# Kernel optimization log

Measured on AMD Instinct MI355X. Metric: run time of the kernel, lower is better.

The kernel has to match this reference:

```python
import jax, jax.numpy as jnp
import numpy as np

N, E, B, D, L = 100000, 600000, 128, 128, 3
BOT = 64
EPS = 1e-5


def _forward(query_x, corpus_x, gin_eps, mlp_W1, mlp_b1, mlp_W2, mlp_b2, bn_gamma, bn_beta,
             pool_G1, pool_g1b, pool_G2, pool_g2b, pool_Wm,
             int_G1, int_g1b, int_G2, int_g2b, int_F1, int_f1b, int_F2, int_f2b,
             sc_G1, sc_g1b, sc_G2, sc_g2b, sc_F1, sc_f1b, sc_F2, sc_f2b,
             query_edge_index, query_graph_idx, corpus_edge_index, corpus_graph_idx, num_graphs):
    def gin(x, ei, l):
        # GINConv: sum of source-node features into targets, plus (1+eps)*self
        agg = jax.ops.segment_sum(x[ei[0]], ei[1], num_segments=x.shape[0])
        h = (1.0 + gin_eps[l]) * x + agg
        h = jax.nn.relu(h @ mlp_W1[l] + mlp_b1[l]) @ mlp_W2[l] + mlp_b2[l]
        mu = h.mean(axis=0)
        var = ((h - mu) ** 2).mean(axis=0)  # biased var (BatchNorm training mode)
        h = (h - mu) * jax.lax.rsqrt(var + EPS) * bn_gamma[l] + bn_beta[l]
        return jax.nn.relu(h)  # dropout p=0.0

    def pool(x, gidx, l):
        coef = jnp.tanh(jax.nn.relu(x @ pool_G1[l] + pool_g1b[l]) @ pool_G2[l] + pool_g2b[l])
        s = (coef + 1.0) * x
        sums = jax.ops.segment_sum(s, gidx, num_segments=num_graphs)
        cnt = jax.ops.segment_sum(jnp.ones((x.shape[0],), x.dtype), gidx, num_segments=num_graphs)
        mean = sums / cnt[:, None]
        gc = jnp.tanh(mean @ pool_Wm[l])  # [B, D]
        node_coef = jax.nn.sigmoid(jnp.sum(s * gc[gidx], axis=1))  # [N]
        return jax.ops.segment_sum(node_coef[:, None] * s, gidx, num_segments=num_graphs)

    def interact(q, c, l):
        comb = jnp.concatenate([q, c], axis=1)  # [B, 2D]
        coef = jax.nn.sigmoid(jax.nn.relu(comb @ int_G1[l] + int_g1b[l]) @ int_G2[l] + int_g2b[l])
        sc = (coef + 1.0) * comb
        return jax.nn.relu(jax.nn.relu(sc @ int_F1[l] + int_f1b[l]) @ int_F2[l] + int_f2b[l])

    qx, cx = query_x, corpus_x
    feats = []
    for l in range(gin_eps.shape[0]):
        qx = gin(qx, query_edge_index, l)
        cx = gin(cx, corpus_edge_index, l)
        feats.append(interact(pool(qx, query_graph_idx, l), pool(cx, corpus_graph_idx, l), l))
    f = jnp.concatenate(feats, axis=1)  # [B, sum(filters)//2]
    coef = jax.nn.sigmoid(jax.nn.relu(f @ sc_G1 + sc_g1b) @ sc_G2 + sc_g2b)
    sf = (coef + 1.0) * f
    return (jax.nn.relu(sf @ sc_F1 + sc_f1b) @ sc_F2 + sc_f2b).squeeze(-1)  # [B]


def setup_inputs() -> dict:
    key = jax.random.key(0)
    kit = iter(jax.random.split(key, 64))
    def nrm(shape, s=0.05):
        return jax.random.normal(next(kit), shape, jnp.float32) * s
    C, R, OUT, AGG, RG = 2 * D, (2 * D) // 4, D // 2, (3 * D) // 2, ((3 * D) // 2) // 4
    inp = {
        "query_x": nrm((N, D), 1.0),
        "query_edge_index": jax.random.randint(next(kit), (2, E), 0, N),
        "query_graph_idx": jnp.sort(jax.random.randint(next(kit), (N,), 0, B)),
        "corpus_x": nrm((N, D), 1.0),
        "corpus_edge_index": jax.random.randint(next(kit), (2, E), 0, N),
        "corpus_graph_idx": jnp.sort(jax.random.randint(next(kit), (N,), 0, B)),
        "num_graphs": B,
        "gin_eps": jnp.zeros((L,), jnp.float32),
        "mlp_W1": nrm((L, D, D)), "mlp_b1": jnp.zeros((L, D)),
        "mlp_W2": nrm((L, D, D)), "mlp_b2": jnp.zeros((L, D)),
        "bn_gamma": jnp.ones((L, D)), "bn_beta": jnp.zeros((L, D)),
        "pool_G1": nrm((L, D, D // 4)), "pool_g1b": jnp.zeros((L, D // 4)),
        "pool_G2": nrm((L, D // 4, D)), "pool_g2b": jnp.zeros((L, D)),
        "pool_Wm": nrm((L, D, D)),
        "int_G1": nrm((L, C, R)), "int_g1b": jnp.zeros((L, R)),
        "int_G2": nrm((L, R, C)), "int_g2b": jnp.zeros((L, C)),
        "int_F1": nrm((L, C, C)), "int_f1b": jnp.zeros((L, C)),
        "int_F2": nrm((L, C, OUT)), "int_f2b": jnp.zeros((L, OUT)),
        "sc_G1": nrm((AGG, RG)), "sc_g1b": jnp.zeros((RG,)),
        "sc_G2": nrm((RG, AGG)), "sc_g2b": jnp.zeros((AGG,)),
        "sc_F1": nrm((AGG, BOT)), "sc_f1b": jnp.zeros((BOT,)),
        "sc_F2": nrm((BOT, 1)), "sc_f2b": jnp.zeros((1,)),
    }
    return inp


def reference(query_x, query_edge_index, query_graph_idx, corpus_x, corpus_edge_index, corpus_graph_idx,
              num_graphs, gin_eps, mlp_W1, mlp_b1, mlp_W2, mlp_b2, bn_gamma, bn_beta,
              pool_G1, pool_g1b, pool_G2, pool_g2b, pool_Wm,
              int_G1, int_g1b, int_G2, int_g2b, int_F1, int_f1b, int_F2, int_f2b,
              sc_G1, sc_g1b, sc_G2, sc_g2b, sc_F1, sc_f1b, sc_F2, sc_f2b):
    return _forward(query_x, corpus_x, gin_eps, mlp_W1, mlp_b1, mlp_W2, mlp_b2, bn_gamma, bn_beta,
                    pool_G1, pool_g1b, pool_G2, pool_g2b, pool_Wm,
                    int_G1, int_g1b, int_G2, int_g2b, int_F1, int_f1b, int_F2, int_f2b,
                    sc_G1, sc_g1b, sc_G2, sc_g2b, sc_F1, sc_f1b, sc_F2, sc_f2b,
                    query_edge_index, query_graph_idx, corpus_edge_index, corpus_graph_idx, num_graphs)
```

## Files before the change

### kernel.cpp

```cpp
#include <hip/hip_runtime.h>
#include <hip/hip_bf16.h>

constexpr int NN  = 100000;
constexpr int NN2 = 200000;
constexpr int NE  = 600000;
constexpr int NB  = 128;
constexpr int D   = 128;
constexpr int NL  = 3;
constexpr int CAP = 48;
constexpr int MT_TOT = NN2 / 16;
constexpr int MT_Q   = NN / 16;

typedef __bf16 bf16x8 __attribute__((ext_vector_type(8)));
typedef float f32x4 __attribute__((ext_vector_type(4)));
typedef unsigned short us8 __attribute__((ext_vector_type(8)));

__device__ __forceinline__ float sigmoidf_(float x) { return 1.0f / (1.0f + __expf(-x)); }
__device__ __forceinline__ unsigned short f2b(float f) {
    __hip_bfloat16 h = __float2bfloat16(f);
    return __builtin_bit_cast(unsigned short, h);
}
__device__ __forceinline__ float b2f(unsigned short u) {
    __hip_bfloat16 h = __builtin_bit_cast(__hip_bfloat16, u);
    return __bfloat162float(h);
}
__device__ __forceinline__ bf16x8 ldfrag(const unsigned short* p) {
    return __builtin_bit_cast(bf16x8, *(const us8*)p);
}

__global__ __launch_bounds__(256) void k_csr_fill(const int* __restrict__ qei, const int* __restrict__ cei,
                                                  int* __restrict__ deg, int* __restrict__ bucket) {
    int e = blockIdx.x * 256 + threadIdx.x;
    int src, dst;
    if (e < NE) {
        src = qei[e]; dst = qei[NE + e];
    } else if (e < 2 * NE) {
        src = cei[e - NE] + NN; dst = cei[NE + (e - NE)] + NN;
    } else return;
    int pos = atomicAdd(&deg[dst], 1);
    if (pos < CAP) bucket[(size_t)dst * CAP + pos] = src;
}

__global__ __launch_bounds__(256) void k_cnt(const int* __restrict__ gq, const int* __restrict__ gc,
                                             float* __restrict__ cnt) {
    __shared__ float h[256];
    for (int i = threadIdx.x; i < 256; i += 256) h[i] = 0.f;
    __syncthreads();
    int total = gridDim.x * 256;
    int tid = blockIdx.x * 256 + threadIdx.x;
    int per = (NN2 + total - 1) / total;
    int r0 = tid * per, r1 = min(r0 + per, NN2);
    if (r0 < r1) {
        int cur = (r0 < NN) ? gq[r0] : 128 + gc[r0 - NN];
        float c = 0.f;
        for (int r = r0; r < r1; ++r) {
            int g = (r < NN) ? gq[r] : 128 + gc[r - NN];
            if (g != cur) { atomicAdd(&h[cur], c); c = 0.f; cur = g; }
            c += 1.f;
        }
        atomicAdd(&h[cur], c);
    }
    __syncthreads();
    for (int i = threadIdx.x; i < 256; i += 256)
        if (h[i] != 0.f) atomicAdd(&cnt[i], h[i]);
}

__global__ __launch_bounds__(256) void k_wprep_all(
    const float* mW1, const float* mW2, const float* pG1, const float* pG2,
    const float* iG1, const float* iG2, const float* iF1, const float* iF2,
    const float* sG1, const float* sG2, const float* sF1,
    unsigned short* W1t, unsigned short* W2t, unsigned short* G1t, unsigned short* G2t,
    unsigned short* iG1t, unsigned short* iG2t, unsigned short* iF1t, unsigned short* iF2t,
    unsigned short* sG1t, unsigned short* sG2t, unsigned short* sF1t) {
    int i = blockIdx.x * 256 + threadIdx.x;
#define SEG(CNT, KK, NN_, SRC, DST)                                              \
    if (i < (CNT)) {                                                             \
        int l = i / ((KK) * (NN_)), r = i % ((KK) * (NN_));                      \
        int n = r / (KK), k = r % (KK);                                          \
        DST[i] = f2b(SRC[(size_t)l * (KK) * (NN_) + (size_t)k * (NN_) + n]);     \
        return;                                                                  \
    }                                                                            \
    i -= (CNT);
    SEG(49152, 128, 128, mW1, W1t)
    SEG(49152, 128, 128, mW2, W2t)
    SEG(12288, 128, 32, pG1, G1t)
    SEG(12288, 32, 128, pG2, G2t)
    SEG(49152, 256, 64, iG1, iG1t)
    SEG(49152, 64, 256, iG2, iG2t)
    SEG(196608, 256, 256, iF1, iF1t)
    SEG(49152, 256, 64, iF2, iF2t)
    SEG(9216, 192, 48, sG1, sG1t)
    if (i < 12288) {
        int n = i / 64, k = i % 64;
        sG2t[i] = (k < 48) ? f2b(sG2[(size_t)k * 192 + n]) : (unsigned short)0;
        return;
    }
    i -= 12288;
    SEG(12288, 192, 64, sF1, sF1t)
#undef SEG
}

template <bool BF16IN>
__global__ __launch_bounds__(256) void k_gather(const float* __restrict__ qx, const float* __restrict__ cx,
                                                const unsigned short* __restrict__ xb, unsigned short* __restrict__ z,
                                                const int* __restrict__ deg, const int* __restrict__ bucket,
                                                const float* __restrict__ eps_p, int l) {
    int r = blockIdx.x * 16 + (threadIdx.x >> 4);
    int c8 = threadIdx.x & 15;
    float e = 1.0f + eps_p[l];
    float a[8];
    const float* base = nullptr; int off = 0;
    if constexpr (BF16IN) {
        us8 v = *(const us8*)(xb + (size_t)r * D + c8 * 8);
#pragma unroll
        for (int j = 0; j < 8; ++j) a[j] = e * b2f(v[j]);
    } else {
        base = (r < NN) ? qx : cx; off = (r < NN) ? 0 : NN;
        float4 v0 = *(const float4*)(base + (size_t)(r - off) * D + c8 * 8);
        float4 v1 = *(const float4*)(base + (size_t)(r - off) * D + c8 * 8 + 4);
        a[0] = e * v0.x; a[1] = e * v0.y; a[2] = e * v0.z; a[3] = e * v0.w;
        a[4] = e * v1.x; a[5] = e * v1.y; a[6] = e * v1.z; a[7] = e * v1.w;
    }
    int d = deg[r]; d = (d < CAP) ? d : CAP;
    const int* bk = bucket + (size_t)r * CAP;
    int i = 0;
    for (; i + 4 <= d; i += 4) {
        int s0 = bk[i], s1 = bk[i + 1], s2 = bk[i + 2], s3 = bk[i + 3];
        if constexpr (BF16IN) {
            us8 u0 = *(const us8*)(xb + (size_t)s0 * D + c8 * 8);
            us8 u1 = *(const us8*)(xb + (size_t)s1 * D + c8 * 8);
            us8 u2 = *(const us8*)(xb + (size_t)s2 * D + c8 * 8);
            us8 u3 = *(const us8*)(xb + (size_t)s3 * D + c8 * 8);
#pragma unroll
            for (int j = 0; j < 8; ++j)
                a[j] += b2f(u0[j]) + b2f(u1[j]) + b2f(u2[j]) + b2f(u3[j]);
        } else {
            const float* p0 = base + (size_t)(s0 - off) * D + c8 * 8;
            const float* p1 = base + (size_t)(s1 - off) * D + c8 * 8;
            const float* p2 = base + (size_t)(s2 - off) * D + c8 * 8;
            const float* p3 = base + (size_t)(s3 - off) * D + c8 * 8;
            float4 w0 = *(const float4*)p0, w0b = *(const float4*)(p0 + 4);
            float4 w1 = *(const float4*)p1, w1b = *(const float4*)(p1 + 4);
            float4 w2 = *(const float4*)p2, w2b = *(const float4*)(p2 + 4);
            float4 w3 = *(const float4*)p3, w3b = *(const float4*)(p3 + 4);
            a[0] += w0.x + w1.x + w2.x + w3.x; a[1] += w0.y + w1.y + w2.y + w3.y;
            a[2] += w0.z + w1.z + w2.z + w3.z; a[3] += w0.w + w1.w + w2.w + w3.w;
            a[4] += w0b.x + w1b.x + w2b.x + w3b.x; a[5] += w0b.y + w1b.y + w2b.y + w3b.y;
            a[6] += w0b.z + w1b.z + w2b.z + w3b.z; a[7] += w0b.w + w1b.w + w2b.w + w3b.w;
        }
    }
    for (; i < d; ++i) {
        int s0 = bk[i];
        if constexpr (BF16IN) {
            us8 u0 = *(const us8*)(xb + (size_t)s0 * D + c8 * 8);
#pragma unroll
            for (int j = 0; j < 8; ++j) a[j] += b2f(u0[j]);
        } else {
            const float* p0 = base + (size_t)(s0 - off) * D + c8 * 8;
            float4 w0 = *(const float4*)p0, w0b = *(const float4*)(p0 + 4);
            a[0] += w0.x; a[1] += w0.y; a[2] += w0.z; a[3] += w0.w;
            a[4] += w0b.x; a[5] += w0b.y; a[6] += w0b.z; a[7] += w0b.w;
        }
    }
    us8 o;
#pragma unroll
    for (int j = 0; j < 8; ++j) o[j] = f2b(a[j]);
    *(us8*)(z + (size_t)r * D + c8 * 8) = o;
}

constexpr int HSTR = 136;
__global__ __launch_bounds__(256, 2) void k_mlp(unsigned short* zh,
                                                const unsigned short* __restrict__ W1t,
                                                const unsigned short* __restrict__ W2t,
                                                const float* __restrict__ b1,
                                                const float* __restrict__ b2,
                                                float* __restrict__ stat) {
    __shared__ unsigned short hb[2][2][16 * HSTR];
    __shared__ float red[512];
    int wave = threadIdx.x >> 6, lane = threadIdx.x & 63;
    int col16 = lane & 15, quad = lane >> 4;
    int g = wave >> 1, half = wave & 1;
    bf16x8 bf1[4][4], bf2[4][4];
    float bb1[4], bb2[4];
#pragma unroll
    for (int t = 0; t < 4; ++t) {
        int c = half * 64 + t * 16 + col16;
        bb1[t] = b1[c]; bb2[t] = b2[c];
#pragma unroll
        for (int kc = 0; kc < 4; ++kc) {
            bf1[t][kc] = ldfrag(W1t + (size_t)c * D + kc * 32 + quad * 8);
            bf2[t][kc] = ldfrag(W2t + (size_t)c * D + kc * 32 + quad * 8);
        }
    }
    float cs[2][4] = {{0.f,0.f,0.f,0.f},{0.f,0.f,0.f,0.f}};
    float cq[2][4] = {{0.f,0.f,0.f,0.f},{0.f,0.f,0.f,0.f}};
    int groups = gridDim.x * 2;
    int iters = (MT_TOT + groups - 1) / groups;
    for (int n = 0; n < iters; ++n) {
        int mt = blockIdx.x * 2 + g + n * groups;
        bool act = (mt < MT_TOT);
        int pp = n & 1;
        unsigned short* hbuf = hb[pp][g];
        {
            const unsigned short* Ap = zh + ((size_t)(act ? mt : 0) * 16 + col16) * D + quad * 8;
            f32x4 acc[4];
#pragma unroll
            for (int t = 0; t < 4; ++t) acc[t] = (f32x4){0.f, 0.f, 0.f, 0.f};
#pragma unroll
            for (int kc = 0; kc < 4; ++kc) {
                bf16x8 af = ldfrag(Ap + kc * 32);
#pragma unroll
                for (int t = 0; t < 4; ++t)
                    acc[t] = __builtin_amdgcn_mfma_f32_16x16x32_bf16(af, bf1[t][kc], acc[t], 0, 0, 0);
            }
#pragma unroll
            for (int t = 0; t < 4; ++t) {
                int c = half * 64 + t * 16 + col16;
#pragma unroll
                for (int r = 0; r < 4; ++r)
                    hbuf[(quad * 4 + r) * HSTR + c] = f2b(fmaxf(acc[t][r] + bb1[t], 0.f));
            }
        }
        __syncthreads();
        {
            f32x4 acc[4];
#pragma unroll
            for (int t = 0; t < 4; ++t) acc[t] = (f32x4){0.f, 0.f, 0.f, 0.f};
#pragma unroll
            for (int kc = 0; kc < 4; ++kc) {
                bf16x8 af = ldfrag(&hbuf[col16 * HSTR + kc * 32 + quad * 8]);
#pragma unroll
                for (int t = 0; t < 4; ++t)
                    acc[t] = __builtin_amdgcn_mfma_f32_16x16x32_bf16(af, bf2[t][kc], acc[t], 0, 0, 0);
            }
            if (act) {
                int side = (mt < MT_Q) ? 0 : 1;
#pragma unroll
                for (int t = 0; t < 4; ++t) {
                    int c = half * 64 + t * 16 + col16;
#pragma unroll
                    for (int r = 0; r < 4; ++r) {
                        int m = mt * 16 + quad * 4 + r;
                        float v = acc[t][r] + bb2[t];
                        zh[(size_t)m * D + c] = f2b(v);
                        cs[side][t] += v; cq[side][t] += v * v;
                    }
                }
            }
        }
    }
    for (int i = threadIdx.x; i < 512; i += 256) red[i] = 0.f;
    __syncthreads();
#pragma unroll
    for (int t = 0; t < 4; ++t) {
        int c = half * 64 + t * 16 + col16;
#pragma unroll
        for (int side = 0; side < 2; ++side) {
            atomicAdd(&red[side * 256 + c], cs[side][t]);
            atomicAdd(&red[side * 256 + 128 + c], cq[side][t]);
        }
    }
    __syncthreads();
    for (int i = threadIdx.x; i < 512; i += 256) atomicAdd(&stat[i], red[i]);
}

__global__ __launch_bounds__(256, 2) void k_pool(const unsigned short* __restrict__ H,
                                                 const unsigned short* __restrict__ G1t,
                                                 const unsigned short* __restrict__ G2t,
                                                 const float* __restrict__ b1,
                                                 const float* __restrict__ b2,
                                                 const float* __restrict__ stat,
                                                 const float* __restrict__ gamma,
                                                 const float* __restrict__ beta,
                                                 const int* __restrict__ gq, const int* __restrict__ gcix,
                                                 unsigned short* __restrict__ Xo,
                                                 unsigned short* __restrict__ S,
                                                 float* __restrict__ seg_sum) {
    __shared__ float sc_s[256], sh_s[256];
    __shared__ unsigned short xt[4][16 * HSTR];
    __shared__ unsigned short t2t[4][16 * 40];
    {
        int t = threadIdx.x, side = t >> 7, c = t & 127;
        const float invN = 1.0f / (float)NN;
        float mu = stat[side * 256 + c] * invN;
        float var = fmaxf(stat[side * 256 + 128 + c] * invN - mu * mu, 0.f);
        float inv = rsqrtf(var + 1e-5f);
        float s = gamma[c] * inv;
        sc_s[t] = s;
        sh_s[t] = beta[c] - mu * s;
    }
    __syncthreads();
    int wave = threadIdx.x >> 6, lane = threadIdx.x & 63;
    int col16 = lane & 15, quad = lane >> 4;
    unsigned short* xtile = xt[wave];
    unsigned short* t2tile = t2t[wave];
    int nwaves = gridDim.x * 4;
    int per = (MT_TOT + nwaves - 1) / nwaves;
    int wid = blockIdx.x * 4 + wave;
    int mt0 = wid * per, mt1 = min(mt0 + per, MT_TOT);
    if (mt0 >= mt1) return;

    bf16x8 g1f[2][4], g2f[8];
    float bb1[2], bb2[8];
#pragma unroll
    for (int t = 0; t < 2; ++t) {
        int c = t * 16 + col16;
        bb1[t] = b1[c];
#pragma unroll
        for (int kc = 0; kc < 4; ++kc)
            g1f[t][kc] = ldfrag(G1t + (size_t)c * D + kc * 32 + quad * 8);
    }
#pragma unroll
    for (int t = 0; t < 8; ++t) {
        int c = t * 16 + col16;
        bb2[t] = b2[c];
        g2f[t] = ldfrag(G2t + (size_t)c * 32 + quad * 8);
    }
    float sacc[8] = {0.f, 0.f, 0.f, 0.f, 0.f, 0.f, 0.f, 0.f};
    int curg = -1;
    for (int mt = mt0; mt < mt1; ++mt) {
        int side = (mt < MT_Q) ? 0 : 1;
        const float* scp = sc_s + side * 128;
        const float* shp = sh_s + side * 128;
        const unsigned short* Hp = H + ((size_t)mt * 16 + col16) * D + quad * 8;
        unsigned short* Xp = Xo + ((size_t)mt * 16 + col16) * D + quad * 8;
        f32x4 acc1[2];
#pragma unroll
        for (int t = 0; t < 2; ++t) acc1[t] = (f32x4){0.f, 0.f, 0.f, 0.f};
#pragma unroll
        for (int kc = 0; kc < 4; ++kc) {
            us8 hv = *(const us8*)(Hp + kc * 32);
            int k0 = kc * 32 + quad * 8;
            float4 s0 = *(const float4*)&scp[k0], s1 = *(const float4*)&scp[k0 + 4];
            float4 h0 = *(const float4*)&shp[k0], h1 = *(const float4*)&shp[k0 + 4];
            us8 xv;
            xv[0] = f2b(fmaxf(b2f(hv[0]) * s0.x + h0.x, 0.f));
            xv[1] = f2b(fmaxf(b2f(hv[1]) * s0.y + h0.y, 0.f));
            xv[2] = f2b(fmaxf(b2f(hv[2]) * s0.z + h0.z, 0.f));
            xv[3] = f2b(fmaxf(b2f(hv[3]) * s0.w + h0.w, 0.f));
            xv[4] = f2b(fmaxf(b2f(hv[4]) * s1.x + h1.x, 0.f));
            xv[5] = f2b(fmaxf(b2f(hv[5]) * s1.y + h1.y, 0.f));
            xv[6] = f2b(fmaxf(b2f(hv[6]) * s1.z + h1.z, 0.f));
            xv[7] = f2b(fmaxf(b2f(hv[7]) * s1.w + h1.w, 0.f));
            *(us8*)(Xp + kc * 32) = xv;
            *(us8*)(xtile + col16 * HSTR + k0) = xv;
            bf16x8 af = __builtin_bit_cast(bf16x8, xv);
#pragma unroll
            for (int t = 0; t < 2; ++t)
                acc1[t] = __builtin_amdgcn_mfma_f32_16x16x32_bf16(af, g1f[t][kc], acc1[t], 0, 0, 0);
        }
#pragma unroll
        for (int t = 0; t < 2; ++t) {
            int c = t * 16 + col16;
#pragma unroll
            for (int r = 0; r < 4; ++r)
                t2tile[(quad * 4 + r) * 40 + c] = f2b(fmaxf(acc1[t][r] + bb1[t], 0.f));
        }
        bf16x8 af2 = ldfrag(t2tile + col16 * 40 + quad * 8);
        f32x4 acc2[8];
#pragma unroll
        for (int t = 0; t < 8; ++t) {
            acc2[t] = (f32x4){0.f, 0.f, 0.f, 0.f};
            acc2[t] = __builtin_amdgcn_mfma_f32_16x16x32_bf16(af2, g2f[t], acc2[t], 0, 0, 0);
        }
#pragma unroll
        for (int r = 0; r < 4; ++r) {
            int m = mt * 16 + quad * 4 + r;
            int g = (m < NN) ? gq[m] : 128 + gcix[m - NN];
            if (g != curg) {
                if (curg >= 0) {
#pragma unroll
                    for (int t = 0; t < 8; ++t) {
                        atomicAdd(&seg_sum[(size_t)curg * D + t * 16 + col16], sacc[t]);
                        sacc[t] = 0.f;
                    }
                }
                curg = g;
            }
#pragma unroll
            for (int t = 0; t < 8; ++t) {
                int c = t * 16 + col16;
                float v = (tanhf(acc2[t][r] + bb2[t]) + 1.f) * b2f(xtile[(quad * 4 + r) * HSTR + c]);
                S[(size_t)m * D + c] = f2b(v);
                sacc[t] += v;
            }
        }
    }
    if (curg >= 0) {
#pragma unroll
        for (int t = 0; t < 8; ++t)
            atomicAdd(&seg_sum[(size_t)curg * D + t * 16 + col16], sacc[t]);
    }
}

__global__ void k_gc(const float* __restrict__ sums, const float* __restrict__ cnt,
                     const float* __restrict__ Wm, float* __restrict__ gc) {
    __shared__ float m[D];
    int b = blockIdx.x, j = threadIdx.x;
    m[j] = sums[b * D + j] / cnt[b];
    __syncthreads();
    float a = 0.f;
#pragma unroll 8
    for (int i = 0; i < D; ++i) a += m[i] * Wm[i * D + j];
    gc[b * D + j] = tanhf(a);
}

__global__ __launch_bounds__(256) void k_ncseg(const unsigned short* __restrict__ S,
                                               const int* __restrict__ gq, const int* __restrict__ gc,
                                               const float* __restrict__ gcb,
                                               float* __restrict__ dq, float* __restrict__ dc) {
    int stream = blockIdx.x * 4 + (threadIdx.x >> 6);
    int lane = threadIdx.x & 63;
    int nstream = gridDim.x * 4;
    int per = (NN2 + nstream - 1) / nstream;
    int r0 = stream * per;
    int r1 = min(r0 + per, NN2);
    if (r0 >= r1) return;
    float a0 = 0.f, a1 = 0.f;
    int cur = (r0 < NN) ? gq[r0] : 128 + gc[r0 - NN];
    for (int r = r0; r < r1; ++r) {
        int g = (r < NN) ? gq[r] : 128 + gc[r - NN];
        if (g != cur) {
            float* base = (cur < 128) ? (dq + cur * D) : (dc + (cur - 128) * D);
            atomicAdd(&base[lane * 2], a0);
            atomicAdd(&base[lane * 2 + 1], a1);
            a0 = 0.f; a1 = 0.f; cur = g;
        }
        ushort2 sv = *(const ushort2*)&S[(size_t)r * D + lane * 2];
        float2 gv = *(const float2*)&gcb[(size_t)g * D + lane * 2];
        float v0 = b2f(sv.x), v1 = b2f(sv.y);
        float p = v0 * gv.x + v1 * gv.y;
#pragma unroll
        for (int off = 1; off < 64; off <<= 1) p += __shfl_xor(p, off, 64);
        float nc = sigmoidf_(p);
        a0 += nc * v0; a1 += nc * v1;
    }
    float* base = (cur < 128) ? (dq + cur * D) : (dc + (cur - 128) * D);
    atomicAdd(&base[lane * 2], a0);
    atomicAdd(&base[lane * 2 + 1], a1);
}

constexpr int LSTR = 264;
__global__ __launch_bounds__(256) void k_interact(const float* __restrict__ pooled,
                                                  const unsigned short* __restrict__ iG1t, const float* __restrict__ ig1b,
                                                  const unsigned short* __restrict__ iG2t, const float* __restrict__ ig2b,
                                                  const unsigned short* __restrict__ iF1t, const float* __restrict__ if1b,
                                                  const unsigned short* __restrict__ iF2t, const float* __restrict__ if2b,
                                                  unsigned short* __restrict__ featsb) {
    __shared__ unsigned short bufC[16 * LSTR];
    __shared__ unsigned short bufA[16 * LSTR];
    __shared__ unsigned short bufB[16 * LSTR];
    int t = threadIdx.x, wave = t >> 6, lane = t & 63;
    int col16 = lane & 15, quad = lane >> 4;
    int pg = blockIdx.x & 7, l = blockIdx.x >> 3;
    int p0 = pg * 16;
    {
        int r = t >> 4, c0 = (t & 15) * 16;
        const float* src = (c0 < 128)
            ? (pooled + (size_t)l * NB * D + (size_t)(p0 + r) * D + c0)
            : (pooled + (size_t)(NL + l) * NB * D + (size_t)(p0 + r) * D + (c0 - 128));
#pragma unroll
        for (int j = 0; j < 16; ++j) bufC[r * LSTR + c0 + j] = f2b(src[j]);
    }
    __syncthreads();
    {
        f32x4 acc = (f32x4){0.f, 0.f, 0.f, 0.f};
        int n = wave * 16 + col16;
#pragma unroll
        for (int kc = 0; kc < 8; ++kc) {
            bf16x8 af = ldfrag(&bufC[col16 * LSTR + kc * 32 + quad * 8]);
            bf16x8 bfr = ldfrag(iG1t + ((size_t)l * 64 + n) * 256 + kc * 32 + quad * 8);
            acc = __builtin_amdgcn_mfma_f32_16x16x32_bf16(af, bfr, acc, 0, 0, 0);
        }
        float bb = ig1b[(size_t)l * 64 + n];
#pragma unroll
        for (int r = 0; r < 4; ++r)
            bufA[(quad * 4 + r) * LSTR + n] = f2b(fmaxf(acc[r] + bb, 0.f));
    }
    __syncthreads();
    {
        f32x4 acc[4];
#pragma unroll
        for (int tt = 0; tt < 4; ++tt) acc[tt] = (f32x4){0.f, 0.f, 0.f, 0.f};
#pragma unroll
        for (int kc = 0; kc < 2; ++kc) {
            bf16x8 af = ldfrag(&bufA[col16 * LSTR + kc * 32 + quad * 8]);
#pragma unroll
            for (int tt = 0; tt < 4; ++tt) {
                int n = wave * 64 + tt * 16 + col16;
                bf16x8 bfr = ldfrag(iG2t + ((size_t)l * 256 + n) * 64 + kc * 32 + quad * 8);
                acc[tt] = __builtin_amdgcn_mfma_f32_16x16x32_bf16(af, bfr, acc[tt], 0, 0, 0);
            }
        }
#pragma unroll
        for (int tt = 0; tt < 4; ++tt) {
            int n = wave * 64 + tt * 16 + col16;
            float bb = ig2b[(size_t)l * 256 + n];
#pragma unroll
            for (int r = 0; r < 4; ++r) {
                int row = quad * 4 + r;
                float s = (sigmoidf_(acc[tt][r] + bb) + 1.f) * b2f(bufC[row * LSTR + n]);
                bufB[row * LSTR + n] = f2b(s);
            }
        }
    }
    __syncthreads();
    {
        f32x4 acc[4];
#pragma unroll
        for (int tt = 0; tt < 4; ++tt) acc[tt] = (f32x4){0.f, 0.f, 0.f, 0.f};
#pragma unroll
        for (int kc = 0; kc < 8; ++kc) {
            bf16x8 af = ldfrag(&bufB[col16 * LSTR + kc * 32 + quad * 8]);
#pragma unroll
            for (int tt = 0; tt < 4; ++tt) {
                int n = wave * 64 + tt * 16 + col16;
                bf16x8 bfr = ldfrag(iF1t + (size_t)l * 256 * 256 + (size_t)n * 256 + kc * 32 + quad * 8);
                acc[tt] = __builtin_amdgcn_mfma_f32_16x16x32_bf16(af, bfr, acc[tt], 0, 0, 0);
            }
        }
#pragma unroll
        for (int tt = 0; tt < 4; ++tt) {
            int n = wave * 64 + tt * 16 + col16;
            float bb = if1b[(size_t)l * 256 + n];
#pragma unroll
            for (int r = 0; r < 4; ++r)
                bufA[(quad * 4 + r) * LSTR + n] = f2b(fmaxf(acc[tt][r] + bb, 0.f));
        }
    }
    __syncthreads();
    {
        f32x4 acc = (f32x4){0.f, 0.f, 0.f, 0.f};
        int n = wave * 16 + col16;
#pragma unroll
        for (int kc = 0; kc < 8; ++kc) {
            bf16x8 af = ldfrag(&bufA[col16 * LSTR + kc * 32 + quad * 8]);
            bf16x8 bfr = ldfrag(iF2t + ((size_t)l * 64 + n) * 256 + kc * 32 + quad * 8);
            acc = __builtin_amdgcn_mfma_f32_16x16x32_bf16(af, bfr, acc, 0, 0, 0);
        }
        float bb = if2b[(size_t)l * 64 + n];
#pragma unroll
        for (int r = 0; r < 4; ++r)
            featsb[(size_t)(p0 + quad * 4 + r) * 192 + l * 64 + n] = f2b(fmaxf(acc[r] + bb, 0.f));
    }
}

__global__ __launch_bounds__(256) void k_score(const unsigned short* __restrict__ featsb,
                                               const unsigned short* __restrict__ sG1t, const float* __restrict__ sg1b,
                                               const unsigned short* __restrict__ sG2t, const float* __restrict__ sg2b,
                                               const unsigned short* __restrict__ sF1t, const float* __restrict__ sf1b,
                                               const float* __restrict__ sF2, const float* __restrict__ sf2b,
                                               float* __restrict__ out) {
    __shared__ unsigned short bufF[16 * 200];
    __shared__ unsigned short bufA[16 * LSTR];
    __shared__ unsigned short bufB[16 * LSTR];
    __shared__ float redf[16 * 65];
    int t = threadIdx.x, wave = t >> 6, lane = t & 63;
    int col16 = lane & 15, quad = lane >> 4;
    int p0 = blockIdx.x * 16;
    {
        int r = t >> 4, c0 = (t & 15) * 12;
#pragma unroll
        for (int j = 0; j < 12; ++j)
            bufF[r * 200 + c0 + j] = featsb[(size_t)(p0 + r) * 192 + c0 + j];
    }
    __syncthreads();
    if (wave < 3) {
        f32x4 acc = (f32x4){0.f, 0.f, 0.f, 0.f};
        int n = wave * 16 + col16;
#pragma unroll
        for (int kc = 0; kc < 6; ++kc) {
            bf16x8 af = ldfrag(&bufF[col16 * 200 + kc * 32 + quad * 8]);
            bf16x8 bfr = ldfrag(sG1t + (size_t)n * 192 + kc * 32 + quad * 8);
            acc = __builtin_amdgcn_mfma_f32_16x16x32_bf16(af, bfr, acc, 0, 0, 0);
        }
        float bb = sg1b[n];
#pragma unroll
        for (int r = 0; r < 4; ++r)
            bufA[(quad * 4 + r) * LSTR + n] = f2b(fmaxf(acc[r] + bb, 0.f));
    } else {
        int row = lane >> 2, c = 48 + (lane & 3) * 4;
#pragma unroll
        for (int j = 0; j < 4; ++j) bufA[row * LSTR + c + j] = 0;
    }
    __syncthreads();
    {
        f32x4 acc[3];
#pragma unroll
        for (int tt = 0; tt < 3; ++tt) acc[tt] = (f32x4){0.f, 0.f, 0.f, 0.f};
#pragma unroll
        for (int kc = 0; kc < 2; ++kc) {
            bf16x8 af = ldfrag(&bufA[col16 * LSTR + kc * 32 + quad * 8]);
#pragma unroll
            for (int tt = 0; tt < 3; ++tt) {
                int n = wave * 48 + tt * 16 + col16;
                bf16x8 bfr = ldfrag(sG2t + (size_t)n * 64 + kc * 32 + quad * 8);
                acc[tt] = __builtin_amdgcn_mfma_f32_16x16x32_bf16(af, bfr, acc[tt], 0, 0, 0);
            }
        }
#pragma unroll
        for (int tt = 0; tt < 3; ++tt) {
            int n = wave * 48 + tt * 16 + col16;
            float bb = sg2b[n];
#pragma unroll
            for (int r = 0; r < 4; ++r) {
                int row = quad * 4 + r;
                float s = (sigmoidf_(acc[tt][r] + bb) + 1.f) * b2f(bufF[row * 200 + n]);
                bufB[row * LSTR + n] = f2b(s);
            }
        }
    }
    __syncthreads();
    {
        f32x4 acc = (f32x4){0.f, 0.f, 0.f, 0.f};
        int n = wave * 16 + col16;
#pragma unroll
        for (int kc = 0; kc < 6; ++kc) {
            bf16x8 af = ldfrag(&bufB[col16 * LSTR + kc * 32 + quad * 8]);
            bf16x8 bfr = ldfrag(sF1t + (size_t)n * 192 + kc * 32 + quad * 8);
            acc = __builtin_amdgcn_mfma_f32_16x16x32_bf16(af, bfr, acc, 0, 0, 0);
        }
        float bb = sf1b[n], w2 = sF2[n];
#pragma unroll
        for (int r = 0; r < 4; ++r)
            redf[(quad * 4 + r) * 65 + n] = fmaxf(acc[r] + bb, 0.f) * w2;
    }
    __syncthreads();
    if (t < 16) {
        float s = 0.f;
#pragma unroll 8
        for (int i = 0; i < 64; ++i) s += redf[t * 65 + i];
        out[p0 + t] = s + sf2b[0];
    }
}

extern "C" void kernel_launch(void* const* d_in, const int* in_sizes, int n_in,
                              void* d_out, int out_size, void* d_ws, size_t ws_size,
                              hipStream_t stream) {
    const float* query_x   = (const float*)d_in[0];
    const int*   query_ei  = (const int*)d_in[1];
    const int*   query_gi  = (const int*)d_in[2];
    const float* corpus_x  = (const float*)d_in[3];
    const int*   corpus_ei = (const int*)d_in[4];
    const int*   corpus_gi = (const int*)d_in[5];
    const float* gin_eps   = (const float*)d_in[7];
    const float* mlp_W1    = (const float*)d_in[8];
    const float* mlp_b1    = (const float*)d_in[9];
    const float* mlp_W2    = (const float*)d_in[10];
    const float* mlp_b2    = (const float*)d_in[11];
    const float* bn_gamma  = (const float*)d_in[12];
    const float* bn_beta   = (const float*)d_in[13];
    const float* pool_G1   = (const float*)d_in[14];
    const float* pool_g1b  = (const float*)d_in[15];
    const float* pool_G2   = (const float*)d_in[16];
    const float* pool_g2b  = (const float*)d_in[17];
    const float* pool_Wm   = (const float*)d_in[18];
    const float* int_G1    = (const float*)d_in[19];
    const float* int_g1b   = (const float*)d_in[20];
    const float* int_G2    = (const float*)d_in[21];
    const float* int_g2b   = (const float*)d_in[22];
    const float* int_F1    = (const float*)d_in[23];
    const float* int_f1b   = (const float*)d_in[24];
    const float* int_F2    = (const float*)d_in[25];
    const float* int_f2b   = (const float*)d_in[26];
    const float* sc_G1     = (const float*)d_in[27];
    const float* sc_g1b    = (const float*)d_in[28];
    const float* sc_G2     = (const float*)d_in[29];
    const float* sc_g2b    = (const float*)d_in[30];
    const float* sc_F1     = (const float*)d_in[31];
    const float* sc_f1b    = (const float*)d_in[32];
    const float* sc_F2     = (const float*)d_in[33];
    const float* sc_f2b    = (const float*)d_in[34];
    float* out = (float*)d_out;

    unsigned short* Zb  = (unsigned short*)d_ws;
    unsigned short* Xb  = Zb + (size_t)NN2 * D;
    unsigned short* Sb  = Xb + (size_t)NN2 * D;
    unsigned short* featsb = Sb + (size_t)NN2 * D;
    unsigned short* W1t = featsb + 128 * 192;
    unsigned short* W2t = W1t + NL * D * D;
    unsigned short* G1t = W2t + NL * D * D;
    unsigned short* G2t = G1t + NL * 32 * D;
    unsigned short* iG1t = G2t + NL * D * 32;
    unsigned short* iG2t = iG1t + NL * 64 * 256;
    unsigned short* iF1t = iG2t + NL * 256 * 64;
    unsigned short* iF2t = iF1t + NL * 256 * 256;
    unsigned short* sG1t = iF2t + NL * 64 * 256;
    unsigned short* sG2t = sG1t + 48 * 192;
    unsigned short* sF1t = sG2t + 192 * 64;
    int* deg    = (int*)(sF1t + 64 * 192);
    int* bucket = deg + NN2;
    float* bn_stat  = (float*)(bucket + (size_t)NN2 * CAP);
    float* seg_sum  = bn_stat + NL * 512;
    float* seg_cnt  = seg_sum + 256 * D;
    float* gcb      = seg_cnt + 256;
    float* pooled   = gcb + 256 * D;

    k_wprep_all<<<1956, 256, 0, stream>>>(mlp_W1, mlp_W2, pool_G1, pool_G2,
                                          int_G1, int_G2, int_F1, int_F2,
                                          sc_G1, sc_G2, sc_F1,
                                          W1t, W2t, G1t, G2t, iG1t, iG2t, iF1t, iF2t,
                                          sG1t, sG2t, sF1t);

    hipMemsetAsync(deg, 0, NN2 * sizeof(int), stream);
    hipMemsetAsync(bn_stat, 0, NL * 512 * sizeof(float), stream);
    hipMemsetAsync(pooled, 0, 2 * NL * NB * D * sizeof(float), stream);
    hipMemsetAsync(seg_cnt, 0, 256 * sizeof(float), stream);
    k_csr_fill<<<(2 * NE + 255) / 256, 256, 0, stream>>>(query_ei, corpus_ei, deg, bucket);
    k_cnt<<<64, 256, 0, stream>>>(query_gi, corpus_gi, seg_cnt);

    for (int l = 0; l < NL; ++l) {
        if (l == 0)
            k_gather<false><<<NN2 / 16, 256, 0, stream>>>(query_x, corpus_x, nullptr, Zb,
                                                          deg, bucket, gin_eps, l);
        else
            k_gather<true><<<NN2 / 16, 256, 0, stream>>>(nullptr, nullptr, Xb, Zb,
                                                         deg, bucket, gin_eps, l);
        k_mlp<<<1024, 256, 0, stream>>>(Zb, W1t + (size_t)l * D * D, W2t + (size_t)l * D * D,
                                        mlp_b1 + l * D, mlp_b2 + l * D, bn_stat + l * 512);
        hipMemsetAsync(seg_sum, 0, 256 * D * sizeof(float), stream);
        k_pool<<<782, 256, 0, stream>>>(Zb, G1t + (size_t)l * 32 * D, G2t + (size_t)l * D * 32,
                                        pool_g1b + l * 32, pool_g2b + l * D,
                                        bn_stat + l * 512, bn_gamma + l * D, bn_beta + l * D,
                                        query_gi, corpus_gi, Xb, Sb, seg_sum);
        k_gc<<<256, D, 0, stream>>>(seg_sum, seg_cnt, pool_Wm + (size_t)l * D * D, gcb);
        k_ncseg<<<1024, 256, 0, stream>>>(Sb, query_gi, corpus_gi, gcb,
                                          pooled + (size_t)l * NB * D,
                                          pooled + (size_t)(NL + l) * NB * D);
    }
    k_interact<<<24, 256, 0, stream>>>(pooled, iG1t, int_g1b, iG2t, int_g2b,
                                       iF1t, int_f1b, iF2t, int_f2b, featsb);
    k_score<<<8, 256, 0, stream>>>(featsb, sG1t, sc_g1b, sG2t, sc_g2b,
                                   sF1t, sc_f1b, sc_F2, sc_f2b, out);
}
```

Before: 1.070 ms.

## Fuse GIN neighbor gather into MLP kernel via shared-memory tile

Merges the neighbor-sum gather kernel and the two-layer MLP kernel into one persistent kernel. Each block gathers a 16-row tile into shared memory, then runs both MFMA GEMMs on it, with the four waves splitting output columns. This avoids writing and re-reading the intermediate Z buffer and drops one launch per layer. In exchange, the gather latency is no longer overlapped across independent blocks, each tile adds an extra barrier, and only one 16-row tile is in flight per block instead of two.

```diff
diff --git a/kernel.cpp b/kernel.cpp
--- a/kernel.cpp
+++ b/kernel.cpp
@@ -100,91 +100,28 @@
 #undef SEG
 }
 
+constexpr int HSTR = 136;
 template <bool BF16IN>
-__global__ __launch_bounds__(256) void k_gather(const float* __restrict__ qx, const float* __restrict__ cx,
-                                                const unsigned short* __restrict__ xb, unsigned short* __restrict__ z,
-                                                const int* __restrict__ deg, const int* __restrict__ bucket,
-                                                const float* __restrict__ eps_p, int l) {
-    int r = blockIdx.x * 16 + (threadIdx.x >> 4);
-    int c8 = threadIdx.x & 15;
-    float e = 1.0f + eps_p[l];
-    float a[8];
-    const float* base = nullptr; int off = 0;
-    if constexpr (BF16IN) {
-        us8 v = *(const us8*)(xb + (size_t)r * D + c8 * 8);
-#pragma unroll
-        for (int j = 0; j < 8; ++j) a[j] = e * b2f(v[j]);
-    } else {
-        base = (r < NN) ? qx : cx; off = (r < NN) ? 0 : NN;
-        float4 v0 = *(const float4*)(base + (size_t)(r - off) * D + c8 * 8);
-        float4 v1 = *(const float4*)(base + (size_t)(r - off) * D + c8 * 8 + 4);
-        a[0] = e * v0.x; a[1] = e * v0.y; a[2] = e * v0.z; a[3] = e * v0.w;
-        a[4] = e * v1.x; a[5] = e * v1.y; a[6] = e * v1.z; a[7] = e * v1.w;
-    }
-    int d = deg[r]; d = (d < CAP) ? d : CAP;
-    const int* bk = bucket + (size_t)r * CAP;
-    int i = 0;
-    for (; i + 4 <= d; i += 4) {
-        int s0 = bk[i], s1 = bk[i + 1], s2 = bk[i + 2], s3 = bk[i + 3];
-        if constexpr (BF16IN) {
-            us8 u0 = *(const us8*)(xb + (size_t)s0 * D + c8 * 8);
-            us8 u1 = *(const us8*)(xb + (size_t)s1 * D + c8 * 8);
-            us8 u2 = *(const us8*)(xb + (size_t)s2 * D + c8 * 8);
-            us8 u3 = *(const us8*)(xb + (size_t)s3 * D + c8 * 8);
-#pragma unroll
-            for (int j = 0; j < 8; ++j)
-                a[j] += b2f(u0[j]) + b2f(u1[j]) + b2f(u2[j]) + b2f(u3[j]);
-        } else {
-            const float* p0 = base + (size_t)(s0 - off) * D + c8 * 8;
-            const float* p1 = base + (size_t)(s1 - off) * D + c8 * 8;
-            const float* p2 = base + (size_t)(s2 - off) * D + c8 * 8;
-            const float* p3 = base + (size_t)(s3 - off) * D + c8 * 8;
-            float4 w0 = *(const float4*)p0, w0b = *(const float4*)(p0 + 4);
-            float4 w1 = *(const float4*)p1, w1b = *(const float4*)(p1 + 4);
-            float4 w2 = *(const float4*)p2, w2b = *(const float4*)(p2 + 4);
-            float4 w3 = *(const float4*)p3, w3b = *(const float4*)(p3 + 4);
-            a[0] += w0.x + w1.x + w2.x + w3.x; a[1] += w0.y + w1.y + w2.y + w3.y;
-            a[2] += w0.z + w1.z + w2.z + w3.z; a[3] += w0.w + w1.w + w2.w + w3.w;
-            a[4] += w0b.x + w1b.x + w2b.x + w3b.x; a[5] += w0b.y + w1b.y + w2b.y + w3b.y;
-            a[6] += w0b.z + w1b.z + w2b.z + w3b.z; a[7] += w0b.w + w1b.w + w2b.w + w3b.w;
-        }
-    }
-    for (; i < d; ++i) {
-        int s0 = bk[i];
-        if constexpr (BF16IN) {
-            us8 u0 = *(const us8*)(xb + (size_t)s0 * D + c8 * 8);
-#pragma unroll
-            for (int j = 0; j < 8; ++j) a[j] += b2f(u0[j]);
-        } else {
-            const float* p0 = base + (size_t)(s0 - off) * D + c8 * 8;
-            float4 w0 = *(const float4*)p0, w0b = *(const float4*)(p0 + 4);
-            a[0] += w0.x; a[1] += w0.y; a[2] += w0.z; a[3] += w0.w;
-            a[4] += w0b.x; a[5] += w0b.y; a[6] += w0b.z; a[7] += w0b.w;
-        }
-    }
-    us8 o;
-#pragma unroll
-    for (int j = 0; j < 8; ++j) o[j] = f2b(a[j]);
-    *(us8*)(z + (size_t)r * D + c8 * 8) = o;
-}
-
-constexpr int HSTR = 136;
-__global__ __launch_bounds__(256, 2) void k_mlp(unsigned short* zh,
-                                                const unsigned short* __restrict__ W1t,
-                                                const unsigned short* __restrict__ W2t,
-                                                const float* __restrict__ b1,
-                                                const float* __restrict__ b2,
-                                                float* __restrict__ stat) {
-    __shared__ unsigned short hb[2][2][16 * HSTR];
+__global__ __launch_bounds__(256, 2) void k_gmlp(const float* __restrict__ qx, const float* __restrict__ cx,
+                                                 const unsigned short* __restrict__ xb,
+                                                 unsigned short* __restrict__ hout,
+                                                 const int* __restrict__ deg, const int* __restrict__ bucket,
+                                                 const float* __restrict__ eps_p, int l,
+                                                 const unsigned short* __restrict__ W1t,
+                                                 const unsigned short* __restrict__ W2t,
+                                                 const float* __restrict__ b1,
+                                                 const float* __restrict__ b2,
+                                                 float* __restrict__ stat) {
+    __shared__ unsigned short zt[16 * HSTR];
+    __shared__ unsigned short ht[16 * HSTR];
     __shared__ float red[512];
     int wave = threadIdx.x >> 6, lane = threadIdx.x & 63;
     int col16 = lane & 15, quad = lane >> 4;
-    int g = wave >> 1, half = wave & 1;
-    bf16x8 bf1[4][4], bf2[4][4];
-    float bb1[4], bb2[4];
-#pragma unroll
-    for (int t = 0; t < 4; ++t) {
-        int c = half * 64 + t * 16 + col16;
+    bf16x8 bf1[2][4], bf2[2][4];
+    float bb1[2], bb2[2];
+#pragma unroll
+    for (int t = 0; t < 2; ++t) {
+        int c = wave * 32 + t * 16 + col16;
         bb1[t] = b1[c]; bb2[t] = b2[c];
 #pragma unroll
         for (int kc = 0; kc < 4; ++kc) {
@@ -192,57 +129,115 @@
             bf2[t][kc] = ldfrag(W2t + (size_t)c * D + kc * 32 + quad * 8);
         }
     }
-    float cs[2][4] = {{0.f,0.f,0.f,0.f},{0.f,0.f,0.f,0.f}};
-    float cq[2][4] = {{0.f,0.f,0.f,0.f},{0.f,0.f,0.f,0.f}};
-    int groups = gridDim.x * 2;
-    int iters = (MT_TOT + groups - 1) / groups;
+    float e = 1.0f + eps_p[l];
+    int gr = threadIdx.x >> 4, c8 = threadIdx.x & 15;
+    float cs[2][2] = {{0.f, 0.f}, {0.f, 0.f}};
+    float cq[2][2] = {{0.f, 0.f}, {0.f, 0.f}};
+    int iters = (MT_TOT + gridDim.x - 1) / gridDim.x;
     for (int n = 0; n < iters; ++n) {
-        int mt = blockIdx.x * 2 + g + n * groups;
+        int mt = blockIdx.x + n * gridDim.x;
         bool act = (mt < MT_TOT);
-        int pp = n & 1;
-        unsigned short* hbuf = hb[pp][g];
-        {
-            const unsigned short* Ap = zh + ((size_t)(act ? mt : 0) * 16 + col16) * D + quad * 8;
-            f32x4 acc[4];
-#pragma unroll
-            for (int t = 0; t < 4; ++t) acc[t] = (f32x4){0.f, 0.f, 0.f, 0.f};
-#pragma unroll
-            for (int kc = 0; kc < 4; ++kc) {
-                bf16x8 af = ldfrag(Ap + kc * 32);
-#pragma unroll
-                for (int t = 0; t < 4; ++t)
-                    acc[t] = __builtin_amdgcn_mfma_f32_16x16x32_bf16(af, bf1[t][kc], acc[t], 0, 0, 0);
-            }
-#pragma unroll
-            for (int t = 0; t < 4; ++t) {
-                int c = half * 64 + t * 16 + col16;
-#pragma unroll
-                for (int r = 0; r < 4; ++r)
-                    hbuf[(quad * 4 + r) * HSTR + c] = f2b(fmaxf(acc[t][r] + bb1[t], 0.f));
-            }
-        }
+        int row = (act ? mt : 0) * 16 + gr;
+        float a[8];
+        const float* base = nullptr; int off = 0;
+        if constexpr (BF16IN) {
+            us8 v = *(const us8*)(xb + (size_t)row * D + c8 * 8);
+#pragma unroll
+            for (int j = 0; j < 8; ++j) a[j] = e * b2f(v[j]);
+        } else {
+            base = (row < NN) ? qx : cx; off = (row < NN) ? 0 : NN;
+            float4 v0 = *(const float4*)(base + (size_t)(row - off) * D + c8 * 8);
+            float4 v1 = *(const float4*)(base + (size_t)(row - off) * D + c8 * 8 + 4);
+            a[0] = e * v0.x; a[1] = e * v0.y; a[2] = e * v0.z; a[3] = e * v0.w;
+            a[4] = e * v1.x; a[5] = e * v1.y; a[6] = e * v1.z; a[7] = e * v1.w;
+        }
+        int d = act ? deg[row] : 0; d = (d < CAP) ? d : CAP;
+        const int* bk = bucket + (size_t)row * CAP;
+        int i = 0;
+        for (; i + 4 <= d; i += 4) {
+            int s0 = bk[i], s1 = bk[i + 1], s2 = bk[i + 2], s3 = bk[i + 3];
+            if constexpr (BF16IN) {
+                us8 u0 = *(const us8*)(xb + (size_t)s0 * D + c8 * 8);
+                us8 u1 = *(const us8*)(xb + (size_t)s1 * D + c8 * 8);
+                us8 u2 = *(const us8*)(xb + (size_t)s2 * D + c8 * 8);
+                us8 u3 = *(const us8*)(xb + (size_t)s3 * D + c8 * 8);
+#pragma unroll
+                for (int j = 0; j < 8; ++j)
+                    a[j] += b2f(u0[j]) + b2f(u1[j]) + b2f(u2[j]) + b2f(u3[j]);
+            } else {
+                const float* p0 = base + (size_t)(s0 - off) * D + c8 * 8;
+                const float* p1 = base + (size_t)(s1 - off) * D + c8 * 8;
+                const float* p2 = base + (size_t)(s2 - off) * D + c8 * 8;
+                const float* p3 = base + (size_t)(s3 - off) * D + c8 * 8;
+                float4 w0 = *(const float4*)p0, w0b = *(const float4*)(p0 + 4);
+                float4 w1 = *(const float4*)p1, w1b = *(const float4*)(p1 + 4);
+                float4 w2 = *(const float4*)p2, w2b = *(const float4*)(p2 + 4);
+                float4 w3 = *(const float4*)p3, w3b = *(const float4*)(p3 + 4);
+                a[0] += w0.x + w1.x + w2.x + w3.x; a[1] += w0.y + w1.y + w2.y + w3.y;
+                a[2] += w0.z + w1.z + w2.z + w3.z; a[3] += w0.w + w1.w + w2.w + w3.w;
+                a[4] += w0b.x + w1b.x + w2b.x + w3b.x; a[5] += w0b.y + w1b.y + w2b.y + w3b.y;
+                a[6] += w0b.z + w1b.z + w2b.z + w3b.z; a[7] += w0b.w + w1b.w + w2b.w + w3b.w;
+            }
+        }
+        for (; i < d; ++i) {
+            int s0 = bk[i];
+            if constexpr (BF16IN) {
+                us8 u0 = *(const us8*)(xb + (size_t)s0 * D + c8 * 8);
+#pragma unroll
+                for (int j = 0; j < 8; ++j) a[j] += b2f(u0[j]);
+            } else {
+                const float* p0 = base + (size_t)(s0 - off) * D + c8 * 8;
+                float4 w0 = *(const float4*)p0, w0b = *(const float4*)(p0 + 4);
+                a[0] += w0.x; a[1] += w0.y; a[2] += w0.z; a[3] += w0.w;
+                a[4] += w0b.x; a[5] += w0b.y; a[6] += w0b.z; a[7] += w0b.w;
+            }
+        }
+        us8 o;
+#pragma unroll
+        for (int j = 0; j < 8; ++j) o[j] = f2b(a[j]);
+        *(us8*)(zt + gr * HSTR + c8 * 8) = o;
         __syncthreads();
         {
-            f32x4 acc[4];
-#pragma unroll
-            for (int t = 0; t < 4; ++t) acc[t] = (f32x4){0.f, 0.f, 0.f, 0.f};
+            f32x4 acc[2];
+#pragma unroll
+            for (int t = 0; t < 2; ++t) acc[t] = (f32x4){0.f, 0.f, 0.f, 0.f};
 #pragma unroll
             for (int kc = 0; kc < 4; ++kc) {
-                bf16x8 af = ldfrag(&hbuf[col16 * HSTR + kc * 32 + quad * 8]);
-#pragma unroll
-                for (int t = 0; t < 4; ++t)
+                bf16x8 af = ldfrag(zt + col16 * HSTR + kc * 32 + quad * 8);
+#pragma unroll
+                for (int t = 0; t < 2; ++t)
+                    acc[t] = __builtin_amdgcn_mfma_f32_16x16x32_bf16(af, bf1[t][kc], acc[t], 0, 0, 0);
+            }
+#pragma unroll
+            for (int t = 0; t < 2; ++t) {
+                int c = wave * 32 + t * 16 + col16;
+#pragma unroll
+                for (int r = 0; r < 4; ++r)
+                    ht[(quad * 4 + r) * HSTR + c] = f2b(fmaxf(acc[t][r] + bb1[t], 0.f));
+            }
+        }
+        __syncthreads();
+        {
+            f32x4 acc[2];
+#pragma unroll
+            for (int t = 0; t < 2; ++t) acc[t] = (f32x4){0.f, 0.f, 0.f, 0.f};
+#pragma unroll
+            for (int kc = 0; kc < 4; ++kc) {
+                bf16x8 af = ldfrag(ht + col16 * HSTR + kc * 32 + quad * 8);
+#pragma unroll
+                for (int t = 0; t < 2; ++t)
                     acc[t] = __builtin_amdgcn_mfma_f32_16x16x32_bf16(af, bf2[t][kc], acc[t], 0, 0, 0);
             }
             if (act) {
                 int side = (mt < MT_Q) ? 0 : 1;
 #pragma unroll
-                for (int t = 0; t < 4; ++t) {
-                    int c = half * 64 + t * 16 + col16;
+                for (int t = 0; t < 2; ++t) {
+                    int c = wave * 32 + t * 16 + col16;
 #pragma unroll
                     for (int r = 0; r < 4; ++r) {
                         int m = mt * 16 + quad * 4 + r;
                         float v = acc[t][r] + bb2[t];
-                        zh[(size_t)m * D + c] = f2b(v);
+                        hout[(size_t)m * D + c] = f2b(v);
                         cs[side][t] += v; cq[side][t] += v * v;
                     }
                 }
@@ -252,8 +247,8 @@
     for (int i = threadIdx.x; i < 512; i += 256) red[i] = 0.f;
     __syncthreads();
 #pragma unroll
-    for (int t = 0; t < 4; ++t) {
-        int c = half * 64 + t * 16 + col16;
+    for (int t = 0; t < 2; ++t) {
+        int c = wave * 32 + t * 16 + col16;
 #pragma unroll
         for (int side = 0; side < 2; ++side) {
             atomicAdd(&red[side * 256 + c], cs[side][t]);
@@ -711,13 +706,15 @@
 
     for (int l = 0; l < NL; ++l) {
         if (l == 0)
-            k_gather<false><<<NN2 / 16, 256, 0, stream>>>(query_x, corpus_x, nullptr, Zb,
-                                                          deg, bucket, gin_eps, l);
+            k_gmlp<false><<<1024, 256, 0, stream>>>(query_x, corpus_x, nullptr, Zb,
+                                                    deg, bucket, gin_eps, l,
+                                                    W1t + (size_t)l * D * D, W2t + (size_t)l * D * D,
+                                                    mlp_b1 + l * D, mlp_b2 + l * D, bn_stat + l * 512);
         else
-            k_gather<true><<<NN2 / 16, 256, 0, stream>>>(nullptr, nullptr, Xb, Zb,
-                                                         deg, bucket, gin_eps, l);
-        k_mlp<<<1024, 256, 0, stream>>>(Zb, W1t + (size_t)l * D * D, W2t + (size_t)l * D * D,
-                                        mlp_b1 + l * D, mlp_b2 + l * D, bn_stat + l * 512);
+            k_gmlp<true><<<1024, 256, 0, stream>>>(nullptr, nullptr, Xb, Zb,
+                                                   deg, bucket, gin_eps, l,
+                                                   W1t + (size_t)l * D * D, W2t + (size_t)l * D * D,
+                                                   mlp_b1 + l * D, mlp_b2 + l * D, bn_stat + l * 512);
         hipMemsetAsync(seg_sum, 0, 256 * D * sizeof(float), stream);
         k_pool<<<782, 256, 0, stream>>>(Zb, G1t + (size_t)l * 32 * D, G2t + (size_t)l * D * 32,
                                         pool_g1b + l * 32, pool_g2b + l * D,
```

Measured after the change: 1.117 ms. 1.04x slower.

## Replace capped bucket adjacency with exact CSR via degree prefix scan

Applied to the files above, without the earlier changes.

The fixed-capacity per-node bucket (CAP=48), which silently dropped edges past the cap, is replaced by a compact CSR built with a degree count, a three-kernel prefix scan and a cursor-based fill. The gather now reads neighbour lists from a contiguous array instead of a sparse 48-slot stride, cutting memory footprint and improving locality. In exchange it adds four small kernel launches and a second atomic pass over the edges. The per-layer seg_sum memset is also folded into k_gc, which zeroes the sums after reading them.

```diff
diff --git a/kernel.cpp b/kernel.cpp
--- a/kernel.cpp
+++ b/kernel.cpp
@@ -7,9 +7,9 @@
 constexpr int NB  = 128;
 constexpr int D   = 128;
 constexpr int NL  = 3;
-constexpr int CAP = 48;
 constexpr int MT_TOT = NN2 / 16;
 constexpr int MT_Q   = NN / 16;
+constexpr int NBLK   = (NN2 + 255) / 256;
 
 typedef __bf16 bf16x8 __attribute__((ext_vector_type(8)));
 typedef float f32x4 __attribute__((ext_vector_type(4)));
@@ -28,8 +28,72 @@
     return __builtin_bit_cast(bf16x8, *(const us8*)p);
 }
 
-__global__ __launch_bounds__(256) void k_csr_fill(const int* __restrict__ qei, const int* __restrict__ cei,
-                                                  int* __restrict__ deg, int* __restrict__ bucket) {
+__global__ __launch_bounds__(256) void k_deg(const int* __restrict__ qei, const int* __restrict__ cei,
+                                             int* __restrict__ deg) {
+    int e = blockIdx.x * 256 + threadIdx.x;
+    int dst;
+    if (e < NE) dst = qei[NE + e];
+    else if (e < 2 * NE) dst = cei[NE + (e - NE)] + NN;
+    else return;
+    atomicAdd(&deg[dst], 1);
+}
+
+__global__ __launch_bounds__(256) void k_scan1(const int* __restrict__ deg, int* __restrict__ bsum) {
+    __shared__ int s[256];
+    int i = blockIdx.x * 256 + threadIdx.x;
+    s[threadIdx.x] = (i < NN2) ? deg[i] : 0;
+    __syncthreads();
+    for (int o = 128; o > 0; o >>= 1) {
+        if (threadIdx.x < o) s[threadIdx.x] += s[threadIdx.x + o];
+        __syncthreads();
+    }
+    if (threadIdx.x == 0) bsum[blockIdx.x] = s[0];
+}
+__global__ __launch_bounds__(256) void k_scan2(int* __restrict__ bsum) {
+    __shared__ int ls[256];
+    int t = threadIdx.x;
+    int v[4]; int loc = 0;
+#pragma unroll
+    for (int j = 0; j < 4; ++j) {
+        int idx = t * 4 + j;
+        v[j] = (idx < NBLK) ? bsum[idx] : 0;
+        loc += v[j];
+    }
+    ls[t] = loc;
+    __syncthreads();
+    for (int o = 1; o < 256; o <<= 1) {
+        int add = (t >= o) ? ls[t - o] : 0;
+        __syncthreads();
+        ls[t] += add;
+        __syncthreads();
+    }
+    int ex = ls[t] - loc;
+#pragma unroll
+    for (int j = 0; j < 4; ++j) {
+        int idx = t * 4 + j;
+        if (idx < NBLK) { int val = v[j]; bsum[idx] = ex; ex += val; }
+    }
+}
+__global__ __launch_bounds__(256) void k_scan3(const int* __restrict__ deg, const int* __restrict__ bsum,
+                                               int* __restrict__ rs, int* __restrict__ cursor) {
+    __shared__ int ls[256];
+    int i = blockIdx.x * 256 + threadIdx.x;
+    int d = (i < NN2) ? deg[i] : 0;
+    ls[threadIdx.x] = d;
+    __syncthreads();
+    for (int o = 1; o < 256; o <<= 1) {
+        int add = (threadIdx.x >= o) ? ls[threadIdx.x - o] : 0;
+        __syncthreads();
+        ls[threadIdx.x] += add;
+        __syncthreads();
+    }
+    int ex = bsum[blockIdx.x] + ls[threadIdx.x] - d;
+    if (i < NN2) { rs[i] = ex; cursor[i] = ex; }
+    if (i == NN2 - 1) rs[NN2] = ex + d;
+}
+
+__global__ __launch_bounds__(256) void k_fill2(const int* __restrict__ qei, const int* __restrict__ cei,
+                                               int* __restrict__ cursor, int* __restrict__ cpt) {
     int e = blockIdx.x * 256 + threadIdx.x;
     int src, dst;
     if (e < NE) {
@@ -37,8 +101,8 @@
     } else if (e < 2 * NE) {
         src = cei[e - NE] + NN; dst = cei[NE + (e - NE)] + NN;
     } else return;
-    int pos = atomicAdd(&deg[dst], 1);
-    if (pos < CAP) bucket[(size_t)dst * CAP + pos] = src;
+    int pos = atomicAdd(&cursor[dst], 1);
+    cpt[pos] = src;
 }
 
 __global__ __launch_bounds__(256) void k_cnt(const int* __restrict__ gq, const int* __restrict__ gc,
@@ -103,7 +167,7 @@
 template <bool BF16IN>
 __global__ __launch_bounds__(256) void k_gather(const float* __restrict__ qx, const float* __restrict__ cx,
                                                 const unsigned short* __restrict__ xb, unsigned short* __restrict__ z,
-                                                const int* __restrict__ deg, const int* __restrict__ bucket,
+                                                const int* __restrict__ rs, const int* __restrict__ cpt,
                                                 const float* __restrict__ eps_p, int l) {
     int r = blockIdx.x * 16 + (threadIdx.x >> 4);
     int c8 = threadIdx.x & 15;
@@ -121,8 +185,9 @@
         a[0] = e * v0.x; a[1] = e * v0.y; a[2] = e * v0.z; a[3] = e * v0.w;
         a[4] = e * v1.x; a[5] = e * v1.y; a[6] = e * v1.z; a[7] = e * v1.w;
     }
-    int d = deg[r]; d = (d < CAP) ? d : CAP;
-    const int* bk = bucket + (size_t)r * CAP;
+    int s = rs[r];
+    int d = rs[r + 1] - s;
+    const int* bk = cpt + s;
     int i = 0;
     for (; i + 4 <= d; i += 4) {
         int s0 = bk[i], s1 = bk[i + 1], s2 = bk[i + 2], s3 = bk[i + 3];
@@ -393,11 +458,12 @@
     }
 }
 
-__global__ void k_gc(const float* __restrict__ sums, const float* __restrict__ cnt,
+__global__ void k_gc(float* __restrict__ sums, const float* __restrict__ cnt,
                      const float* __restrict__ Wm, float* __restrict__ gc) {
     __shared__ float m[D];
     int b = blockIdx.x, j = threadIdx.x;
     m[j] = sums[b * D + j] / cnt[b];
+    sums[b * D + j] = 0.f;
     __syncthreads();
     float a = 0.f;
 #pragma unroll 8
@@ -688,9 +754,12 @@
     unsigned short* sG1t = iF2t + NL * 64 * 256;
     unsigned short* sG2t = sG1t + 48 * 192;
     unsigned short* sF1t = sG2t + 192 * 64;
-    int* deg    = (int*)(sF1t + 64 * 192);
-    int* bucket = deg + NN2;
-    float* bn_stat  = (float*)(bucket + (size_t)NN2 * CAP);
+    int* deg     = (int*)(sF1t + 64 * 192);
+    int* rs      = deg + NN2;
+    int* cursor  = rs + NN2 + 1;
+    int* cpt     = cursor + NN2;
+    int* bsum    = cpt + 2 * NE;
+    float* bn_stat  = (float*)(bsum + 1024);
     float* seg_sum  = bn_stat + NL * 512;
     float* seg_cnt  = seg_sum + 256 * D;
     float* gcb      = seg_cnt + 256;
@@ -706,19 +775,24 @@
     hipMemsetAsync(bn_stat, 0, NL * 512 * sizeof(float), stream);
     hipMemsetAsync(pooled, 0, 2 * NL * NB * D * sizeof(float), stream);
     hipMemsetAsync(seg_cnt, 0, 256 * sizeof(float), stream);
-    k_csr_fill<<<(2 * NE + 255) / 256, 256, 0, stream>>>(query_ei, corpus_ei, deg, bucket);
+    hipMemsetAsync(seg_sum, 0, 256 * D * sizeof(float), stream);
+
+    k_deg<<<(2 * NE + 255) / 256, 256, 0, stream>>>(query_ei, corpus_ei, deg);
+    k_scan1<<<NBLK, 256, 0, stream>>>(deg, bsum);
+    k_scan2<<<1, 256, 0, stream>>>(bsum);
+    k_scan3<<<NBLK, 256, 0, stream>>>(deg, bsum, rs, cursor);
+    k_fill2<<<(2 * NE + 255) / 256, 256, 0, stream>>>(query_ei, corpus_ei, cursor, cpt);
     k_cnt<<<64, 256, 0, stream>>>(query_gi, corpus_gi, seg_cnt);
 
     for (int l = 0; l < NL; ++l) {
         if (l == 0)
             k_gather<false><<<NN2 / 16, 256, 0, stream>>>(query_x, corpus_x, nullptr, Zb,
-                                                          deg, bucket, gin_eps, l);
+                                                          rs, cpt, gin_eps, l);
         else
             k_gather<true><<<NN2 / 16, 256, 0, stream>>>(nullptr, nullptr, Xb, Zb,
-                                                         deg, bucket, gin_eps, l);
+                                                         rs, cpt, gin_eps, l);
         k_mlp<<<1024, 256, 0, stream>>>(Zb, W1t + (size_t)l * D * D, W2t + (size_t)l * D * D,
                                         mlp_b1 + l * D, mlp_b2 + l * D, bn_stat + l * 512);
-        hipMemsetAsync(seg_sum, 0, 256 * D * sizeof(float), stream);
         k_pool<<<782, 256, 0, stream>>>(Zb, G1t + (size_t)l * 32 * D, G2t + (size_t)l * D * 32,
                                         pool_g1b + l * 32, pool_g2b + l * D,
                                         bn_stat + l * 512, bn_gamma + l * D, bn_beta + l * D,
```

After: 1.162 ms. 1.09x slower.
